# Performance work log

Hardware: AMD Instinct MI355X
Metric: run time of the kernel (lower is better)

Reference implementation:

```python
import jax, jax.numpy as jnp
import numpy as np

EMBD_DIM = 1024
NUM_HEADS = 16
HEAD_DIM = EMBD_DIM // NUM_HEADS


def setup_inputs() -> dict:
    key = jax.random.key(0)
    ks = jax.random.split(key, 9)
    B, S, D = 2, 2048, EMBD_DIM
    scale = 1.0 / np.sqrt(D)
    return {
        "x": jax.random.normal(ks[0], (B, S, D), dtype=jnp.float32),
        "wq": jax.random.normal(ks[1], (D, D), dtype=jnp.float32) * scale,
        "bq": jnp.zeros((D,), dtype=jnp.float32),
        "wk": jax.random.normal(ks[2], (D, D), dtype=jnp.float32) * scale,
        "bk": jnp.zeros((D,), dtype=jnp.float32),
        "wv": jax.random.normal(ks[3], (D, D), dtype=jnp.float32) * scale,
        "bv": jnp.zeros((D,), dtype=jnp.float32),
        "wo": jax.random.normal(ks[4], (D, D), dtype=jnp.float32) * scale,
        "bo": jnp.zeros((D,), dtype=jnp.float32),
    }


def reference(x, wq, bq, wk, bk, wv, bv, wo, bo):
    B, S, D = x.shape
    H, hd = NUM_HEADS, HEAD_DIM
    # projections: weights stored as (in, out) so y = x @ w + b
    q = (x @ wq + bq).reshape(B, S, H, hd).transpose(0, 2, 1, 3)  # [B,H,S,hd]
    k = (x @ wk + bk).reshape(B, S, H, hd).transpose(0, 2, 1, 3)
    v = (x @ wv + bv).reshape(B, S, H, hd).transpose(0, 2, 1, 3)
    scores = jnp.einsum("bhqd,bhkd->bhqk", q, k) / jnp.sqrt(jnp.float32(hd))
    causal = jnp.tril(jnp.ones((S, S), dtype=bool))  # [S,S]
    neg = jnp.finfo(scores.dtype).min
    scores = jnp.where(causal[None, None, :, :], scores, neg)
    attn = jax.nn.softmax(scores, axis=-1)
    out = jnp.einsum("bhqk,bhkd->bhqd", attn, v)  # [B,H,S,hd]
    out = out.transpose(0, 2, 1, 3).reshape(B, S, D)
    return out @ wo + bo
```

## Files before the change

kernel.cpp:

```cpp
#include <hip/hip_runtime.h>
#include <math.h>

#define S_LEN 2048
#define BATCH 2
#define DMODEL 1024
#define NHEADS 16
#define MROWS 4096

typedef short bf8 __attribute__((ext_vector_type(8)));
typedef short bf4 __attribute__((ext_vector_type(4)));
typedef float f32x4 __attribute__((ext_vector_type(4)));
typedef unsigned short u16;

static __device__ inline u16 f2bf(float f) {
    union { float f; unsigned u; } v; v.f = f;
    unsigned r = v.u + 0x7fffu + ((v.u >> 16) & 1u);
    return (u16)(r >> 16);
}

static __device__ inline void load16(const void* g, void* l) {
    __builtin_amdgcn_global_load_lds(
        (const __attribute__((address_space(1))) unsigned int*)g,
        (__attribute__((address_space(3))) unsigned int*)l, 16, 0, 0);
}

__global__ __launch_bounds__(256) void prep_kernel(
    const float* __restrict__ x, u16* __restrict__ xb,
    const float* __restrict__ W0, const float* __restrict__ W1,
    const float* __restrict__ W2, const float* __restrict__ W3,
    u16* __restrict__ wT) {
    const int bx = blockIdx.x, t = threadIdx.x;
    if (bx < 2048) {
        int i = bx * 256 + t;
        const float4* p = (const float4*)x + (size_t)i * 2;
        float4 a = p[0], b = p[1];
        u16 tmp[8] = {f2bf(a.x), f2bf(a.y), f2bf(a.z), f2bf(a.w),
                      f2bf(b.x), f2bf(b.y), f2bf(b.z), f2bf(b.w)};
        ((uint4*)xb)[i] = *(uint4*)tmp;
        return;
    }
    __shared__ u16 Ls[64][65];
    const int id = bx - 2048;
    const int z = id >> 8, rem = id & 255;
    const int n0 = (rem & 15) * 64, k0 = (rem >> 4) * 64;
    const float* W = z == 0 ? W0 : z == 1 ? W1 : z == 2 ? W2 : W3;
    u16* Wt = wT + (size_t)z * 1024 * 1024;
    const int r = t >> 2, c4 = (t & 3) * 16;
    const float* p = W + (size_t)(k0 + r) * 1024 + n0 + c4;
#pragma unroll
    for (int i = 0; i < 16; i += 4) {
        float4 v = *(const float4*)(p + i);
        Ls[r][c4 + i + 0] = f2bf(v.x);
        Ls[r][c4 + i + 1] = f2bf(v.y);
        Ls[r][c4 + i + 2] = f2bf(v.z);
        Ls[r][c4 + i + 3] = f2bf(v.w);
    }
    __syncthreads();
    u16 tmp[16];
#pragma unroll
    for (int i = 0; i < 16; i++) tmp[i] = Ls[c4 + i][r];
    uint4* q = (uint4*)(Wt + (size_t)(n0 + r) * 1024 + k0 + c4);
    q[0] = *(uint4*)tmp;
    q[1] = *(uint4*)(tmp + 8);
}

template <int MODE>
__global__ __launch_bounds__(256) void gemm_mfma(
    const u16* __restrict__ A, const u16* __restrict__ Bt,
    const float* __restrict__ bqp, const float* __restrict__ bkp,
    const float* __restrict__ bvp,
    u16* __restrict__ qout, u16* __restrict__ kout, u16* __restrict__ vtout,
    float* __restrict__ fout, float qscale) {
    __shared__ __align__(16) u16 As[128 * 64];
    __shared__ __align__(16) u16 Bs[128 * 64];

    const int t = threadIdx.x, lane = t & 63, w = t >> 6;
    const int quad = lane >> 4, l16 = lane & 15;
    const int wr = w >> 1, wc = w & 1;
    const int row0 = blockIdx.y * 128, col0 = blockIdx.x * 128;
    const int K = DMODEL;

    const int srow = t >> 3;
    const int ksw = ((t & 7) ^ (srow & 7)) * 8;
    const u16* ag = A + (size_t)(row0 + srow) * K + ksw;
    const u16* bg = Bt + (size_t)(col0 + srow) * K + ksw;
    const int swz = l16 & 7;

    f32x4 acc[4][4] = {};

    u16* lA = As + (size_t)(w * 8) * 64;
    u16* lB = Bs + (size_t)(w * 8) * 64;

    for (int it = 0; it < 16; ++it) {
        if (it) __syncthreads();
        const int k0 = it * 64;
#pragma unroll
        for (int i = 0; i < 4; i++) {
            load16(ag + (size_t)i * 32 * K + k0, lA + i * 32 * 64);
            load16(bg + (size_t)i * 32 * K + k0, lB + i * 32 * 64);
        }
        __syncthreads();
#pragma unroll
        for (int kc = 0; kc < 2; kc++) {
            bf8 xf[4], wf[4];
#pragma unroll
            for (int ni = 0; ni < 4; ni++)
                xf[ni] = *(const bf8*)&As[(wr * 64 + ni * 16 + l16) * 64 +
                                          ((kc * 4 + quad) ^ swz) * 8];
#pragma unroll
            for (int mi = 0; mi < 4; mi++)
                wf[mi] = *(const bf8*)&Bs[(wc * 64 + mi * 16 + l16) * 64 +
                                          ((kc * 4 + quad) ^ swz) * 8];
#pragma unroll
            for (int mi = 0; mi < 4; mi++)
#pragma unroll
                for (int ni = 0; ni < 4; ni++)
                    acc[mi][ni] = __builtin_amdgcn_mfma_f32_16x16x32_bf16(
                        wf[mi], xf[ni], acc[mi][ni], 0, 0, 0);
        }
    }

    const int sect = (col0 + wc * 64) >> 10;
#pragma unroll
    for (int mi = 0; mi < 4; mi++) {
        const int featb = col0 + wc * 64 + mi * 16 + quad * 4;
        float b4[4];
#pragma unroll
        for (int reg = 0; reg < 4; reg++)
            b4[reg] = (MODE == 1 ? bqp : (sect == 0 ? bqp : sect == 1 ? bkp : bvp))
                          [(featb + reg) & 1023];
#pragma unroll
        for (int ni = 0; ni < 4; ni++) {
            const int xrow = row0 + wr * 64 + ni * 16 + l16;
            if (MODE == 1) {
                float4 o;
                o.x = acc[mi][ni][0] + b4[0];
                o.y = acc[mi][ni][1] + b4[1];
                o.z = acc[mi][ni][2] + b4[2];
                o.w = acc[mi][ni][3] + b4[3];
                *(float4*)(fout + (size_t)xrow * 1024 + featb) = o;
            } else {
                const int cf = featb & 1023;
                if (sect == 0) {
                    u16 t4[4];
#pragma unroll
                    for (int reg = 0; reg < 4; reg++)
                        t4[reg] = f2bf((acc[mi][ni][reg] + b4[reg]) * qscale);
                    *(uint2*)(qout + (size_t)xrow * 1024 + cf) = *(uint2*)t4;
                } else if (sect == 1) {
                    u16 t4[4];
#pragma unroll
                    for (int reg = 0; reg < 4; reg++)
                        t4[reg] = f2bf(acc[mi][ni][reg] + b4[reg]);
                    *(uint2*)(kout + (size_t)xrow * 1024 + cf) = *(uint2*)t4;
                } else {
#pragma unroll
                    for (int reg = 0; reg < 4; reg++)
                        vtout[((size_t)(xrow >> 11) * 1024 + cf + reg) * S_LEN +
                              (xrow & 2047)] = f2bf(acc[mi][ni][reg] + b4[reg]);
                }
            }
        }
    }
}

__global__ __launch_bounds__(256) void attn_kernel(const u16* __restrict__ Qg,
                                                   const u16* __restrict__ Kg,
                                                   const u16* __restrict__ Vt,
                                                   u16* __restrict__ Og) {
    __shared__ __align__(16) u16 Ks[2][64][32];
    __shared__ __align__(16) u16 Vs[2][64][32];

    const int t = threadIdx.x, lane = t & 63, w = t >> 6;
    const int quad = lane >> 4, l16 = lane & 15;
    const int qt = 31 - blockIdx.y;
    const int bh = blockIdx.x, b = bh >> 4, h = bh & 15;
    const size_t base = (size_t)b * S_LEN * DMODEL + h * 64;
    const size_t vbase = ((size_t)b * 1024 + h * 64) * S_LEN;
    const int sr = t >> 2, sc = (t & 3) * 16;
    const int pl = sc >> 5;
    const int g0 = (sc >> 3) & 3;
    const int ss = (sr >> 1) & 3;
    const int swz = (l16 >> 1) & 3;

    const u16* kp = Kg + base + (size_t)sr * DMODEL + sc;
    const u16* vp = Vt + vbase + (size_t)sr * S_LEN + sc;
    uint4 k0r = *(const uint4*)kp, k1r = *(const uint4*)(kp + 8);
    uint4 v0r = *(const uint4*)vp, v1r = *(const uint4*)(vp + 8);

    const int niter = qt + 1;
    const int q0 = qt * 64;

    bf8 aq[2];
#pragma unroll
    for (int c = 0; c < 2; c++)
        aq[c] = *(const bf8*)(Qg + base +
            (size_t)(q0 + w * 16 + l16) * DMODEL + c * 32 + quad * 8);

    float lsum = 0.f;
    f32x4 oT[4] = {};

    for (int kt = 0; kt < niter; kt++) {
        __syncthreads();
        *(uint4*)&Ks[pl][sr][(g0 ^ ss) * 8] = k0r;
        *(uint4*)&Ks[pl][sr][((g0 + 1) ^ ss) * 8] = k1r;
        *(uint4*)&Vs[pl][sr][(g0 ^ ss) * 8] = v0r;
        *(uint4*)&Vs[pl][sr][((g0 + 1) ^ ss) * 8] = v1r;
        __syncthreads();
        if (kt + 1 < niter) {
            size_t ok = (size_t)(kt + 1) * 64 * DMODEL;
            int ov = (kt + 1) * 64;
            k0r = *(const uint4*)(kp + ok); k1r = *(const uint4*)(kp + ok + 8);
            v0r = *(const uint4*)(vp + ov); v1r = *(const uint4*)(vp + ov + 8);
        }

        f32x4 scv[4] = {};
        __builtin_amdgcn_s_setprio(1);
#pragma unroll
        for (int c = 0; c < 2; c++)
#pragma unroll
            for (int ns = 0; ns < 4; ns++) {
                bf8 ak = *(const bf8*)&Ks[c][ns * 16 + l16][(quad ^ swz) * 8];
                scv[ns] = __builtin_amdgcn_mfma_f32_16x16x32_bf16(
                    ak, aq[c], scv[ns], 0, 0, 0);
            }
        __builtin_amdgcn_s_setprio(0);

        const bool diag = (kt == qt);
        const int ql = w * 16 + l16;
#pragma unroll
        for (int ns = 0; ns < 4; ns++) {
            float p[4];
#pragma unroll
            for (int r = 0; r < 4; r++) {
                int key = ns * 16 + quad * 4 + r;
                p[r] = (diag && key > ql) ? 0.f
                                          : __builtin_amdgcn_exp2f(scv[ns][r]);
                lsum += p[r];
            }
            union { unsigned u[2]; bf4 v; } pk;
            pk.u[0] = (__float_as_uint(p[0]) >> 16) |
                      (__float_as_uint(p[1]) & 0xffff0000u);
            pk.u[1] = (__float_as_uint(p[2]) >> 16) |
                      (__float_as_uint(p[3]) & 0xffff0000u);
            __builtin_amdgcn_s_setprio(1);
#pragma unroll
            for (int ds = 0; ds < 4; ds++) {
                bf4 av = *(const bf4*)&Vs[ns >> 1][ds * 16 + l16]
                    [((((ns & 1) * 2 + (quad >> 1)) ^ swz) * 8) + (quad & 1) * 4];
                oT[ds] = __builtin_amdgcn_mfma_f32_16x16x16bf16_1k(
                    av, pk.v, oT[ds], 0, 0, 0);
            }
            __builtin_amdgcn_s_setprio(0);
        }
    }

    float l = lsum;
    l += __shfl_xor(l, 16, 64);
    l += __shfl_xor(l, 32, 64);
    const float inv = 1.f / l;
    const int qq = q0 + w * 16 + l16;
#pragma unroll
    for (int ds = 0; ds < 4; ds++) {
        u16 t4[4];
#pragma unroll
        for (int r = 0; r < 4; r++) t4[r] = f2bf(oT[ds][r] * inv);
        *(uint2*)(Og + base + (size_t)qq * DMODEL + ds * 16 + quad * 4) =
            *(uint2*)t4;
    }
}

extern "C" void kernel_launch(void* const* d_in, const int* in_sizes, int n_in,
                              void* d_out, int out_size, void* d_ws, size_t ws_size,
                              hipStream_t stream) {
    const float* x  = (const float*)d_in[0];
    const float* wq = (const float*)d_in[1];
    const float* bq = (const float*)d_in[2];
    const float* wk = (const float*)d_in[3];
    const float* bk = (const float*)d_in[4];
    const float* wv = (const float*)d_in[5];
    const float* bv = (const float*)d_in[6];
    const float* wo = (const float*)d_in[7];
    const float* bo = (const float*)d_in[8];
    float* out = (float*)d_out;

    const size_t E = (size_t)MROWS * DMODEL;
    u16* xb  = (u16*)d_out;
    u16* vt  = xb + E;
    u16* wT  = (u16*)d_ws;
    u16* woT = wT + 3145728;
    u16* qb  = wT + 4194304;
    u16* kb  = qb + E;
    u16* ob  = kb + E;

    dim3 blk(256);
    prep_kernel<<<3072, blk, 0, stream>>>(x, xb, wq, wk, wv, wo, wT);

    gemm_mfma<0><<<dim3(24, 32), blk, 0, stream>>>(
        xb, wT, bq, bk, bv, qb, kb, vt, nullptr, 0.18033688011112042f);

    dim3 agrid(BATCH * NHEADS, 32);
    attn_kernel<<<agrid, blk, 0, stream>>>(qb, kb, vt, ob);

    gemm_mfma<1><<<dim3(8, 32), blk, 0, stream>>>(
        ob, woT, bo, nullptr, nullptr, nullptr, nullptr, nullptr, out, 1.0f);
}
```

Before: 191.5 us.

## Enlarge attention blocks to 128 queries and 128-key tiles with 512 threads

The attention kernel now runs 8 waves per block over 128 query rows and stages 128 keys per iteration. Half the threads load K and half load V into larger shared buffers. This roughly halves the K/V global-to-LDS traffic per query and the number of barrier-separated iterations. In exchange, the first 64-query wave group computes the fully masked upper half of the diagonal tile, which is wasted work. Per-wave register pressure also rises with 8 score accumulators, and the grid shrinks to half as many blocks.

```diff
diff --git a/kernel.cpp b/kernel.cpp
--- a/kernel.cpp
+++ b/kernel.cpp
@@ -164,78 +164,87 @@
     }
 }
 
-__global__ __launch_bounds__(256) void attn_kernel(const u16* __restrict__ Qg,
-                                                   const u16* __restrict__ Kg,
-                                                   const u16* __restrict__ Vt,
-                                                   u16* __restrict__ Og) {
-    __shared__ __align__(16) u16 Ks[2][64][32];
-    __shared__ __align__(16) u16 Vs[2][64][32];
+__global__ __launch_bounds__(512, 4) void attn_kernel(
+    const u16* __restrict__ Qg, const u16* __restrict__ Kg,
+    const u16* __restrict__ Vt, u16* __restrict__ Og) {
+    __shared__ __align__(16) u16 Ks[2][128][32];
+    __shared__ __align__(16) u16 Vs[4][64][32];
 
     const int t = threadIdx.x, lane = t & 63, w = t >> 6;
     const int quad = lane >> 4, l16 = lane & 15;
-    const int qt = 31 - blockIdx.y;
+    const int wtile = w >> 2, wq = w & 3;
+    const int pi = 15 - blockIdx.y;
     const int bh = blockIdx.x, b = bh >> 4, h = bh & 15;
     const size_t base = (size_t)b * S_LEN * DMODEL + h * 64;
     const size_t vbase = ((size_t)b * 1024 + h * 64) * S_LEN;
-    const int sr = t >> 2, sc = (t & 3) * 16;
+
+    const int tl = t & 255;
+    const bool isK = t < 256;
+    const int sr = tl >> 2, sc = (tl & 3) * 16;
     const int pl = sc >> 5;
     const int g0 = (sc >> 3) & 3;
     const int ss = (sr >> 1) & 3;
     const int swz = (l16 >> 1) & 3;
 
-    const u16* kp = Kg + base + (size_t)sr * DMODEL + sc;
-    const u16* vp = Vt + vbase + (size_t)sr * S_LEN + sc;
-    uint4 k0r = *(const uint4*)kp, k1r = *(const uint4*)(kp + 8);
-    uint4 v0r = *(const uint4*)vp, v1r = *(const uint4*)(vp + 8);
-
-    const int niter = qt + 1;
-    const int q0 = qt * 64;
+    const u16* gp = isK ? (Kg + base + (size_t)sr * DMODEL + sc)
+                        : (Vt + vbase + (size_t)sr * S_LEN + sc);
+    const size_t rs = isK ? (size_t)DMODEL : (size_t)1;
+    u16* d0 = isK ? &Ks[pl][sr][0] : &Vs[pl][sr][0];
+    u16* d1 = isK ? &Ks[pl][64 + sr][0] : &Vs[2 + pl][sr][0];
+    const int oa = (g0 ^ ss) * 8, ob2 = ((g0 + 1) ^ ss) * 8;
+
+    uint4 r0a = *(const uint4*)gp, r0b = *(const uint4*)(gp + 8);
+    uint4 r1a = *(const uint4*)(gp + 64 * rs), r1b = *(const uint4*)(gp + 64 * rs + 8);
+
+    const int niter = pi + 1;
+    const int q0 = pi * 128 + wtile * 64;
 
     bf8 aq[2];
 #pragma unroll
     for (int c = 0; c < 2; c++)
         aq[c] = *(const bf8*)(Qg + base +
-            (size_t)(q0 + w * 16 + l16) * DMODEL + c * 32 + quad * 8);
+            (size_t)(q0 + wq * 16 + l16) * DMODEL + c * 32 + quad * 8);
 
     float lsum = 0.f;
     f32x4 oT[4] = {};
 
     for (int kt = 0; kt < niter; kt++) {
         __syncthreads();
-        *(uint4*)&Ks[pl][sr][(g0 ^ ss) * 8] = k0r;
-        *(uint4*)&Ks[pl][sr][((g0 + 1) ^ ss) * 8] = k1r;
-        *(uint4*)&Vs[pl][sr][(g0 ^ ss) * 8] = v0r;
-        *(uint4*)&Vs[pl][sr][((g0 + 1) ^ ss) * 8] = v1r;
+        *(uint4*)(d0 + oa) = r0a;
+        *(uint4*)(d0 + ob2) = r0b;
+        *(uint4*)(d1 + oa) = r1a;
+        *(uint4*)(d1 + ob2) = r1b;
         __syncthreads();
         if (kt + 1 < niter) {
-            size_t ok = (size_t)(kt + 1) * 64 * DMODEL;
-            int ov = (kt + 1) * 64;
-            k0r = *(const uint4*)(kp + ok); k1r = *(const uint4*)(kp + ok + 8);
-            v0r = *(const uint4*)(vp + ov); v1r = *(const uint4*)(vp + ov + 8);
-        }
-
-        f32x4 scv[4] = {};
+            const u16* np = gp + (size_t)(kt + 1) * 128 * rs;
+            r0a = *(const uint4*)np;
+            r0b = *(const uint4*)(np + 8);
+            r1a = *(const uint4*)(np + 64 * rs);
+            r1b = *(const uint4*)(np + 64 * rs + 8);
+        }
+
+        f32x4 scv[8] = {};
         __builtin_amdgcn_s_setprio(1);
 #pragma unroll
         for (int c = 0; c < 2; c++)
 #pragma unroll
-            for (int ns = 0; ns < 4; ns++) {
+            for (int ns = 0; ns < 8; ns++) {
                 bf8 ak = *(const bf8*)&Ks[c][ns * 16 + l16][(quad ^ swz) * 8];
                 scv[ns] = __builtin_amdgcn_mfma_f32_16x16x32_bf16(
                     ak, aq[c], scv[ns], 0, 0, 0);
             }
         __builtin_amdgcn_s_setprio(0);
 
-        const bool diag = (kt == qt);
-        const int ql = w * 16 + l16;
-#pragma unroll
-        for (int ns = 0; ns < 4; ns++) {
+        const bool diag = (kt == niter - 1);
+        const int qloc = wtile * 64 + wq * 16 + l16;
+#pragma unroll
+        for (int ns = 0; ns < 8; ns++) {
             float p[4];
 #pragma unroll
             for (int r = 0; r < 4; r++) {
                 int key = ns * 16 + quad * 4 + r;
-                p[r] = (diag && key > ql) ? 0.f
-                                          : __builtin_amdgcn_exp2f(scv[ns][r]);
+                p[r] = (diag && key > qloc) ? 0.f
+                                            : __builtin_amdgcn_exp2f(scv[ns][r]);
                 lsum += p[r];
             }
             union { unsigned u[2]; bf4 v; } pk;
@@ -259,7 +268,7 @@
     l += __shfl_xor(l, 16, 64);
     l += __shfl_xor(l, 32, 64);
     const float inv = 1.f / l;
-    const int qq = q0 + w * 16 + l16;
+    const int qq = q0 + wq * 16 + l16;
 #pragma unroll
     for (int ds = 0; ds < 4; ds++) {
         u16 t4[4];
@@ -299,8 +308,8 @@
     gemm_mfma<0><<<dim3(24, 32), blk, 0, stream>>>(
         xb, wT, bq, bk, bv, qb, kb, vt, nullptr, 0.18033688011112042f);
 
-    dim3 agrid(BATCH * NHEADS, 32);
-    attn_kernel<<<agrid, blk, 0, stream>>>(qb, kb, vt, ob);
+    attn_kernel<<<dim3(BATCH * NHEADS, 16), dim3(512), 0, stream>>>(
+        qb, kb, vt, ob);
 
     gemm_mfma<1><<<dim3(8, 32), blk, 0, stream>>>(
         ob, woT, bo, nullptr, nullptr, nullptr, nullptr, nullptr, out, 1.0f);
```

Result: no change. 192.6 us (+0.6%).
